# Kernel tuning notes

Measured on AMD Instinct MI355X. Metric: run time of the kernel, lower is better.

## Reference

```python
import jax, jax.numpy as jnp
import numpy as np

NUM_GROUPS = 32
EPS = 1e-6


def setup_inputs() -> dict:
    key = jax.random.key(0)
    ks = jax.random.split(key, 4)
    B, C, H, W = 16, 512, 32, 32
    x = jax.random.normal(ks[0], (B, C, H, W), dtype=jnp.float32)
    norm_w = jnp.ones((C,), dtype=jnp.float32)
    norm_b = jnp.zeros((C,), dtype=jnp.float32)
    qkv_w = jax.random.normal(ks[1], (3 * C, C), dtype=jnp.float32) * (1.0 / np.sqrt(C))
    qkv_b = jnp.zeros((3 * C,), dtype=jnp.float32)
    proj_w = jax.random.normal(ks[2], (C, C), dtype=jnp.float32) * (1.0 / np.sqrt(C))
    proj_b = jnp.zeros((C,), dtype=jnp.float32)
    return {"x": x, "norm_w": norm_w, "norm_b": norm_b, "qkv_w": qkv_w,
            "qkv_b": qkv_b, "proj_w": proj_w, "proj_b": proj_b}


def _group_norm(x, w, b):
    B, C, H, W = x.shape
    g = NUM_GROUPS
    xg = x.reshape(B, g, C // g, H * W)
    mu = xg.mean(axis=(2, 3), keepdims=True)
    var = xg.var(axis=(2, 3), keepdims=True)
    xn = (xg - mu) * jax.lax.rsqrt(var + EPS)
    xn = xn.reshape(B, C, H, W)
    return xn * w[None, :, None, None] + b[None, :, None, None]


def reference(x, norm_w, norm_b, qkv_w, qkv_b, proj_w, proj_b):
    B, C, H, W = x.shape
    h = _group_norm(x, norm_w, norm_b)
    # 1x1 conv == channel GEMM
    qkv = jnp.einsum('oc,bchw->bohw', qkv_w, h) + qkv_b[None, :, None, None]
    q, k, v = jnp.split(qkv, 3, axis=1)
    N = H * W
    q = q.reshape(B, C, N)  # (b, c, n)
    k = k.reshape(B, C, N)
    v = v.reshape(B, C, N)
    scale = jnp.asarray(C, x.dtype) ** -0.5
    attn = jnp.einsum('bci,bcj->bij', q, k) * scale  # (b, Nq, Nk)
    attn = jax.nn.softmax(attn, axis=2)
    o = jnp.einsum('bcj,bij->bci', v, attn).reshape(B, C, H, W)
    out = jnp.einsum('oc,bchw->bohw', proj_w, o) + proj_b[None, :, None, None]
    return x + out
```

## Files before the change

### kernel.cpp

```cpp
#include <hip/hip_runtime.h>

typedef unsigned short u16;
typedef __bf16 bf16x8 __attribute__((ext_vector_type(8)));
typedef float f32x4 __attribute__((ext_vector_type(4)));

#define AS1 __attribute__((address_space(1)))
#define AS3 __attribute__((address_space(3)))


__device__ __forceinline__ u16 f2bf(float f) {
  union { float f; unsigned u; } v; v.f = f;
  return (u16)((v.u + 0x7fffu + ((v.u >> 16) & 1u)) >> 16);
}

__device__ __forceinline__ f32x4 mfma16(bf16x8 a, bf16x8 b, f32x4 c) {
  return __builtin_amdgcn_mfma_f32_16x16x32_bf16(a, b, c, 0, 0, 0);
}

__device__ __forceinline__ void stage_tile(const u16* __restrict__ src, size_t ld,
                                           u16* lds, int wv, int lane) {
#pragma unroll
  for (int h2 = 0; h2 < 2; h2++) {
    int rbase = wv * 32 + h2 * 16;
    int row = rbase + (lane >> 2);
    int segd = (lane & 3) ^ ((row >> 1) & 3);
    __builtin_amdgcn_global_load_lds(
        (const AS1 void*)(src + (size_t)row * ld + segd * 8),
        (AS3 void*)(lds + rbase * 32), 16, 0, 0);
  }
}

__device__ __forceinline__ bf16x8 ldsfrag(const u16* lds, int row, int rowq) {
  int q = rowq ^ ((row >> 1) & 3);
  return *(const bf16x8*)(lds + row * 32 + q * 8);
}

template<int NT>
__device__ __forceinline__ void gemm_core2(const u16* __restrict__ A, int lda,
                                           const u16* __restrict__ B, int ldb,
                                           u16* lds, f32x4 (&acc)[4][4],
                                           int wave, int lane) {
  u16* sA0 = lds;        u16* sA1 = lds + 4096;
  u16* sB0 = lds + 8192; u16* sB1 = lds + 12288;
  int wm = wave >> 1, wn = wave & 1;
  int col = lane & 15, rq = lane >> 4;
#pragma unroll
  for (int m = 0; m < 4; m++)
#pragma unroll
    for (int n = 0; n < 4; n++) acc[m][n] = (f32x4){0.f, 0.f, 0.f, 0.f};

  stage_tile(A, lda, sA0, wave, lane);
  stage_tile(B, ldb, sB0, wave, lane);
  stage_tile(A + 32, lda, sA1, wave, lane);
  stage_tile(B + 32, ldb, sB1, wave, lane);

  for (int t = 0; t < NT; t++) {
    u16* cA = (t & 1) ? sA1 : sA0;
    u16* cB = (t & 1) ? sB1 : sB0;
    if (t < NT - 1) {
      asm volatile("s_waitcnt vmcnt(4)" ::: "memory");
    } else {
      asm volatile("s_waitcnt vmcnt(0)" ::: "memory");
    }
    __builtin_amdgcn_sched_barrier(0);
    __builtin_amdgcn_s_barrier();
    __builtin_amdgcn_sched_barrier(0);
    bf16x8 af[4], bfr[4];
#pragma unroll
    for (int n = 0; n < 4; n++) bfr[n] = ldsfrag(cB, wn * 64 + n * 16 + col, rq);
#pragma unroll
    for (int m = 0; m < 4; m++) af[m] = ldsfrag(cA, wm * 64 + m * 16 + col, rq);
#pragma unroll
    for (int m = 0; m < 4; m++)
#pragma unroll
      for (int n = 0; n < 4; n++) acc[m][n] = mfma16(af[m], bfr[n], acc[m][n]);
    __builtin_amdgcn_sched_barrier(0);
    __builtin_amdgcn_s_barrier();
    if (t + 2 < NT) {
      stage_tile(A + (size_t)(t + 2) * 32, lda, cA, wave, lane);
      stage_tile(B + (size_t)(t + 2) * 32, ldb, cB, wave, lane);
    }
  }
}

__device__ __forceinline__ void stage_half(const u16* __restrict__ src, size_t ld,
                                           u16* ldsbase, int wave, int lane) {
#pragma unroll
  for (int r = 0; r < 2; r++) {
    int rb = (r * 8 + wave) * 8;
    int row = rb + (lane >> 3);
    int seg = (lane & 7) ^ (row & 7);
    __builtin_amdgcn_global_load_lds(
        (const AS1 void*)(src + (size_t)row * ld + seg * 8),
        (AS3 void*)(ldsbase + rb * 64), 16, 0, 0);
  }
}

template<int P>
__device__ __forceinline__ void phase_read(const u16* cA, const u16* cB,
                                           bf16x8 (&af)[2][2], bf16x8 (&bfr)[4][2],
                                           int wm, int wn, int col, int rq) {
  if constexpr (P == 0) {
#pragma unroll
    for (int nf = 0; nf < 4; nf++)
#pragma unroll
      for (int kk = 0; kk < 2; kk++) {
        int row = wn * 64 + nf * 16 + col;
        bfr[nf][kk] = *(const bf16x8*)(cB + row * 64 + (((kk << 2) + rq) ^ (row & 7)) * 8);
      }
  }
#pragma unroll
  for (int i = 0; i < 2; i++)
#pragma unroll
    for (int kk = 0; kk < 2; kk++) {
      int row = wm * 128 + (P * 2 + i) * 16 + col;
      af[i][kk] = *(const bf16x8*)(cA + row * 64 + (((kk << 2) + rq) ^ (row & 7)) * 8);
    }
}

template<int P>
__device__ __forceinline__ void phase_fma(const bf16x8 (&af)[2][2],
                                          const bf16x8 (&bfr)[4][2],
                                          f32x4 (&acc)[8][4]) {
#pragma unroll
  for (int i = 0; i < 2; i++)
#pragma unroll
    for (int kk = 0; kk < 2; kk++)
#pragma unroll
      for (int nf = 0; nf < 4; nf++)
        acc[P * 2 + i][nf] = mfma16(af[i][kk], bfr[nf][kk], acc[P * 2 + i][nf]);
}

#define RUN_PHASE(P, STAGE_CODE, WAIT_CODE)                                  \
  {                                                                          \
    bf16x8 af[2][2];                                                         \
    phase_read<P>(cA, cB, af, bfr, wm, wn, col, rq);                         \
    STAGE_CODE;                                                              \
    WAIT_CODE;                                                               \
    __builtin_amdgcn_sched_barrier(0);                                       \
    __builtin_amdgcn_s_barrier();                                            \
    __builtin_amdgcn_sched_barrier(0);                                       \
    __builtin_amdgcn_s_setprio(1);                                           \
    phase_fma<P>(af, bfr, acc);                                              \
    __builtin_amdgcn_s_setprio(0);                                           \
    __builtin_amdgcn_sched_barrier(0);                                       \
    __builtin_amdgcn_s_barrier();                                            \
    __builtin_amdgcn_sched_barrier(0);                                       \
  }

template<int NT>
__device__ __forceinline__ void gemm8_core(const u16* __restrict__ A, int lda,
                                           const u16* __restrict__ B, int ldb,
                                           u16* lds, f32x4 (&acc)[8][4],
                                           int wave, int lane) {
  u16* Abuf[2] = {lds, lds + 16384};
  u16* Bbuf[2] = {lds + 32768, lds + 49152};
  int wm = wave >> 2, wn = wave & 3;
  int col = lane & 15, rq = lane >> 4;
#pragma unroll
  for (int m = 0; m < 8; m++)
#pragma unroll
    for (int n = 0; n < 4; n++) acc[m][n] = (f32x4){0.f, 0.f, 0.f, 0.f};

  stage_half(A, lda, Abuf[0], wave, lane);
  stage_half(A + 128 * (size_t)lda, lda, Abuf[0] + 8192, wave, lane);
  stage_half(B, ldb, Bbuf[0], wave, lane);
  stage_half(B + 128 * (size_t)ldb, ldb, Bbuf[0] + 8192, wave, lane);
  stage_half(B + 64, ldb, Bbuf[1], wave, lane);
  stage_half(B + 64 + 128 * (size_t)ldb, ldb, Bbuf[1] + 8192, wave, lane);
  asm volatile("s_waitcnt vmcnt(4)" ::: "memory");
  __builtin_amdgcn_sched_barrier(0);
  __builtin_amdgcn_s_barrier();
  __builtin_amdgcn_sched_barrier(0);

  for (int kt = 0; kt < NT; kt++) {
    const u16* cA = Abuf[kt & 1];
    const u16* cB = Bbuf[kt & 1];
    u16* nA = Abuf[(kt + 1) & 1];
    u16* nB = Bbuf[kt & 1];
    const u16* Asrc = A + (size_t)(kt + 1) * 64;
    const u16* Bsrc = B + (size_t)(kt + 2) * 64;
    bool pa = (kt + 1 < NT), pb = (kt + 2 < NT);
    bf16x8 bfr[4][2];
    RUN_PHASE(0, if (pa) stage_half(Asrc, lda, nA, wave, lane), );
    RUN_PHASE(1, if (pa) stage_half(Asrc + 128 * (size_t)lda, lda, nA + 8192, wave, lane), );
    RUN_PHASE(2, if (pb) stage_half(Bsrc, ldb, nB, wave, lane), );
    RUN_PHASE(3, if (pb) stage_half(Bsrc + 128 * (size_t)ldb, ldb, nB + 8192, wave, lane),
              if (pb) { asm volatile("s_waitcnt vmcnt(4)" ::: "memory"); }
              else    { asm volatile("s_waitcnt vmcnt(0)" ::: "memory"); });
  }
}

__global__ __launch_bounds__(256) void gn_fused(const float* __restrict__ x,
                                                const float* __restrict__ gw,
                                                const float* __restrict__ gb,
                                                u16* __restrict__ h) {
  __shared__ float buf[16 * 1032];
  __shared__ float ls[4], lss[4];
  int bg = blockIdx.x;
  int b = bg >> 5, g = bg & 31;
  const float4* p = (const float4*)(x + (size_t)bg * 16384);
  float s = 0.f, ss = 0.f;
  for (int i = threadIdx.x; i < 4096; i += 256) {
    float4 v = p[i];
    int c = i >> 8, n = (i & 255) * 4;
    *(float4*)&buf[c * 1032 + n] = v;
    s  += v.x + v.y + v.z + v.w;
    ss += v.x*v.x + v.y*v.y + v.z*v.z + v.w*v.w;
  }
  for (int d = 32; d; d >>= 1) { s += __shfl_down(s, d); ss += __shfl_down(ss, d); }
  int wv = threadIdx.x >> 6;
  if ((threadIdx.x & 63) == 0) { ls[wv] = s; lss[wv] = ss; }
  __syncthreads();
  float m = (ls[0] + ls[1] + ls[2] + ls[3]) * (1.f / 16384.f);
  float var = (lss[0] + lss[1] + lss[2] + lss[3]) * (1.f / 16384.f) - m * m;
  float r = rsqrtf(var + 1e-6f);
  int c0 = g * 16;
  float w[16], bb[16];
#pragma unroll
  for (int c = 0; c < 16; c++) {
    w[c] = gw[c0 + c] * r;
    bb[c] = gb[c0 + c] - m * w[c];
  }
  for (int n = threadIdx.x; n < 1024; n += 256) {
    u16 o[16];
#pragma unroll
    for (int c = 0; c < 16; c++) o[c] = f2bf(buf[c * 1032 + n] * w[c] + bb[c]);
    u16* dst = h + (((size_t)((b << 10) | n)) << 9) + c0;
    *(uint4*)dst = *(uint4*)o;
    *(uint4*)(dst + 8) = *(uint4*)(o + 8);
  }
}

__global__ __launch_bounds__(256) void cast_w(const float* __restrict__ qkv_w,
                                              const float* __restrict__ proj_w,
                                              u16* __restrict__ wq,
                                              u16* __restrict__ wp) {
  int bid = blockIdx.x;
  const float* src = (bid < 768) ? qkv_w : proj_w;
  u16* dst = (bid < 768) ? wq : wp;
  int base = (bid < 768) ? bid * 1024 : (bid - 768) * 1024;
  int i = base + threadIdx.x * 4;
  float4 v = *(const float4*)(src + i);
  dst[i] = f2bf(v.x); dst[i+1] = f2bf(v.y); dst[i+2] = f2bf(v.z); dst[i+3] = f2bf(v.w);
}

__global__ __launch_bounds__(512, 1) void gemm8_qkv(const u16* __restrict__ A,
                                                    const u16* __restrict__ Bn,
                                                    const float* __restrict__ bias,
                                                    u16* __restrict__ q_nc,
                                                    u16* __restrict__ k_nc,
                                                    u16* __restrict__ v) {
  __shared__ u16 lds[65536];
  int bid = blockIdx.x;
  int xcd = bid & 7, r = bid >> 3;
  int mb = r % 6, nb = xcd * 8 + r / 6;
  int m0 = mb * 256, n0 = nb * 256;
  int t = threadIdx.x, wave = t >> 6, lane = t & 63;
  int wm = wave >> 2, wn = wave & 3;
  int col = lane & 15, rq = lane >> 4;
  f32x4 acc[8][4];
  gemm8_core<8>(A + (size_t)m0 * 512, 512, Bn + (size_t)n0 * 512, 512,
                lds, acc, wave, lane);
  if (mb < 4) {
    u16* dst = (mb < 2) ? q_nc : k_nc;
#pragma unroll
    for (int mf = 0; mf < 8; mf++)
#pragma unroll
      for (int nf = 0; nf < 4; nf++) {
        int o = m0 + wm * 128 + mf * 16 + rq * 4;
        int bn = n0 + wn * 64 + nf * 16 + col;
        u16 tmp[4];
#pragma unroll
        for (int rr = 0; rr < 4; rr++) tmp[rr] = f2bf(acc[mf][nf][rr] + bias[o + rr]);
        *(uint2*)(dst + (size_t)bn * 512 + (o & 511)) = *(uint2*)tmp;
      }
  } else {
#pragma unroll
    for (int mf = 0; mf < 8; mf++)
#pragma unroll
      for (int nf = 0; nf < 4; nf++)
#pragma unroll
        for (int rr = 0; rr < 4; rr++) {
          int o = m0 + wm * 128 + mf * 16 + rq * 4 + rr;
          int bn = n0 + wn * 64 + nf * 16 + col;
          v[(size_t)(o & 511) * 16384 + bn] = f2bf(acc[mf][nf][rr] + bias[o]);
        }
  }
}

__global__ __launch_bounds__(512, 1) void gemm8_s(const u16* __restrict__ q_nc,
                                                  const u16* __restrict__ k_nc,
                                                  u16* __restrict__ E,
                                                  float* __restrict__ part) {
  __shared__ u16 lds[65536];
  int bid = blockIdx.x;
  int xcd = bid & 7, r = bid >> 3;
  int b = xcd * 2 + (r & 1);
  int tile = r >> 1;
  int m0 = (tile >> 2) * 256, n0 = (tile & 3) * 256;
  int t = threadIdx.x, wave = t >> 6, lane = t & 63;
  int wm = wave >> 2, wn = wave & 3;
  int col = lane & 15, rq = lane >> 4;
  f32x4 acc[8][4];
  gemm8_core<8>(q_nc + ((size_t)(b * 1024 + m0)) * 512, 512,
                k_nc + ((size_t)(b * 1024 + n0)) * 512, 512,
                lds, acc, wave, lane);
  u16* Eb = E + ((size_t)b << 20);
  float* pb = part + ((size_t)b << 14);
  int idx = (n0 >> 6) + wn;
  const float scale = 0.04419417382415922f;
#pragma unroll
  for (int mf = 0; mf < 8; mf++)
#pragma unroll
    for (int rr = 0; rr < 4; rr++) {
      float e[4], rs = 0.f;
#pragma unroll
      for (int nf = 0; nf < 4; nf++) { e[nf] = __expf(acc[mf][nf][rr] * scale); rs += e[nf]; }
      rs += __shfl_xor(rs, 1); rs += __shfl_xor(rs, 2);
      rs += __shfl_xor(rs, 4); rs += __shfl_xor(rs, 8);
      int row = m0 + wm * 128 + mf * 16 + rq * 4 + rr;
      if (col == 0) pb[row * 16 + idx] = rs;
#pragma unroll
      for (int nf = 0; nf < 4; nf++) {
        int jj = n0 + wn * 64 + nf * 16 + col;
        Eb[(size_t)row * 1024 + jj] = f2bf(e[nf]);
      }
    }
}

__global__ __launch_bounds__(256) void row_inv2(const float* __restrict__ part,
                                                float* __restrict__ inv) {
  int row = blockIdx.x * 256 + threadIdx.x;
  const float4* p = (const float4*)(part + (size_t)row * 16);
  float4 a = p[0], b = p[1], c = p[2], d = p[3];
  float s = a.x+a.y+a.z+a.w + b.x+b.y+b.z+b.w + c.x+c.y+c.z+c.w + d.x+d.y+d.z+d.w;
  inv[row] = 1.f / s;
}

__global__ __launch_bounds__(256) void gemm_pv(const u16* __restrict__ E,
                                               const u16* __restrict__ v,
                                               const float* __restrict__ inv,
                                               u16* __restrict__ o_nc) {
  __shared__ u16 lds[16384];
  int bid = blockIdx.x;
  int xcd = bid & 7, r = bid >> 3;
  int b = xcd * 2 + (r & 1);
  int tile = r >> 1;
  int m0 = (tile >> 2) * 128, n0 = (tile & 3) * 128;
  int t = threadIdx.x, wave = t >> 6, lane = t & 63;
  int wm = wave >> 1, wn = wave & 1;
  int col = lane & 15, rq = lane >> 4;
  f32x4 acc[4][4];
  gemm_core2<32>(E + ((size_t)b << 20) + (size_t)m0 * 1024, 1024,
                 v + (size_t)n0 * 16384 + ((size_t)b << 10), 16384,
                 lds, acc, wave, lane);
#pragma unroll
  for (int i = 0; i < 4; i++)
#pragma unroll
    for (int rr = 0; rr < 4; rr++) {
      int ii = m0 + wm * 64 + i * 16 + rq * 4 + rr;
      float sc = inv[(b << 10) + ii];
#pragma unroll
      for (int j = 0; j < 4; j++) {
        int cc = n0 + wn * 64 + j * 16 + col;
        o_nc[(((size_t)(b * 1024 + ii)) << 9) + cc] = f2bf(acc[i][j][rr] * sc);
      }
    }
}

__global__ __launch_bounds__(256) void gemm_proj(const u16* __restrict__ A,
                                                 const u16* __restrict__ Bn,
                                                 const float* __restrict__ bias,
                                                 const float* __restrict__ xres,
                                                 float* __restrict__ outp) {
  __shared__ u16 lds[16384];
  int bid = blockIdx.x;
  int xcd = bid & 7, r = bid >> 3;
  int mb = r & 3, nb = xcd * 16 + (r >> 2);
  int m0 = mb * 128, n0 = nb * 128;
  int t = threadIdx.x, wave = t >> 6, lane = t & 63;
  int wm = wave >> 1, wn = wave & 1;
  int col = lane & 15, rq = lane >> 4;
  f32x4 acc[4][4];
  gemm_core2<16>(A + (size_t)m0 * 512, 512, Bn + (size_t)n0 * 512, 512,
                 lds, acc, wave, lane);
#pragma unroll
  for (int i = 0; i < 4; i++)
#pragma unroll
    for (int j = 0; j < 4; j++)
#pragma unroll
      for (int rr = 0; rr < 4; rr++) {
        int co = m0 + wm * 64 + i * 16 + rq * 4 + rr;
        int bn = n0 + wn * 64 + j * 16 + col;
        int bb = bn >> 10, n = bn & 1023;
        size_t oi = (((size_t)(bb * 512 + co)) << 10) + n;
        outp[oi] = acc[i][j][rr] + bias[co] + xres[oi];
      }
}

extern "C" void kernel_launch(void* const* d_in, const int* in_sizes, int n_in,
                              void* d_out, int out_size, void* d_ws, size_t ws_size,
                              hipStream_t stream) {
  const float* x      = (const float*)d_in[0];
  const float* norm_w = (const float*)d_in[1];
  const float* norm_b = (const float*)d_in[2];
  const float* qkv_w  = (const float*)d_in[3];
  const float* qkv_b  = (const float*)d_in[4];
  const float* proj_w = (const float*)d_in[5];
  const float* proj_b = (const float*)d_in[6];
  float* out = (float*)d_out;

  char* ws = (char*)d_ws;
  size_t off = 0;
  auto alloc = [&](size_t bytes) {
    void* p = ws + off;
    off += (bytes + 255) & ~(size_t)255;
    return p;
  };
  float* part = (float*)alloc((size_t)16384 * 16 * 4);
  float* inv  = (float*)alloc(16384 * 4);
  u16* wq   = (u16*)alloc((size_t)1536 * 512 * 2);
  u16* wp   = (u16*)alloc((size_t)512 * 512 * 2);
  u16* h    = (u16*)alloc((size_t)16384 * 512 * 2);
  u16* q_nc = (u16*)alloc((size_t)16384 * 512 * 2);
  u16* k_nc = (u16*)alloc((size_t)16384 * 512 * 2);
  u16* v    = (u16*)alloc((size_t)512 * 16384 * 2);
  u16* E    = (u16*)alloc((size_t)16 * 1024 * 1024 * 2);
  u16* o_nc = h;
  (void)in_sizes; (void)n_in; (void)out_size; (void)ws_size;

  gn_fused<<<512, 256, 0, stream>>>(x, norm_w, norm_b, h);
  cast_w<<<1024, 256, 0, stream>>>(qkv_w, proj_w, wq, wp);
  gemm8_qkv<<<384, 512, 0, stream>>>(wq, h, qkv_b, q_nc, k_nc, v);
  gemm8_s<<<256, 512, 0, stream>>>(q_nc, k_nc, E, part);
  row_inv2<<<64, 256, 0, stream>>>(part, inv);
  gemm_pv<<<512, 256, 0, stream>>>(E, v, inv, o_nc);
  gemm_proj<<<512, 256, 0, stream>>>(wp, o_nc, proj_b, x, out);
}
```

Baseline: 138.6 us.

## Fuse weight cast and row-inverse kernels, stage GEMM epilogues through LDS

Folds the bf16 weight cast into the group-norm kernel and the softmax row-sum inversion into the PV GEMM, which removes two kernel launches. The QKV GEMM moves from 256x256 tiles with 512 threads to 128x128 tiles with 256 threads at higher occupancy. The QKV, S, and PV epilogues now stage results in LDS (padded or XOR-swizzled) and write them out as coalesced 16-byte stores instead of scattered 2-byte or 8-byte stores. The cost is extra LDS traffic and barriers, plus smaller QKV tiles that give less data reuse.

```diff
diff --git a/kernel.cpp b/kernel.cpp
--- a/kernel.cpp
+++ b/kernel.cpp
@@ -80,6 +80,16 @@
       stage_tile(A + (size_t)(t + 2) * 32, lda, cA, wave, lane);
       stage_tile(B + (size_t)(t + 2) * 32, ldb, cB, wave, lane);
     }
+  }
+}
+
+__device__ __forceinline__ void epi_flush(const u16* lds, u16* gdst, size_t stride, int t) {
+#pragma unroll
+  for (int pass = 0; pass < 8; pass++) {
+    int row = pass * 16 + (t >> 4);
+    int ch = (t & 15) * 8;
+    uint4 w = *(const uint4*)(lds + row * 132 + ch);
+    *(uint4*)(gdst + (size_t)row * stride + ch) = w;
   }
 }
 
@@ -194,7 +204,11 @@
 __global__ __launch_bounds__(256) void gn_fused(const float* __restrict__ x,
                                                 const float* __restrict__ gw,
                                                 const float* __restrict__ gb,
-                                                u16* __restrict__ h) {
+                                                const float* __restrict__ qkv_w,
+                                                const float* __restrict__ proj_w,
+                                                u16* __restrict__ h,
+                                                u16* __restrict__ wq,
+                                                u16* __restrict__ wp) {
   __shared__ float buf[16 * 1032];
   __shared__ float ls[4], lss[4];
   int bg = blockIdx.x;
@@ -208,6 +222,20 @@
     s  += v.x + v.y + v.z + v.w;
     ss += v.x*v.x + v.y*v.y + v.z*v.z + v.w*v.w;
   }
+  {
+    int qb = bg * 384;
+    for (int u = threadIdx.x; u < 384; u += 256) {
+      float4 v = *(const float4*)(qkv_w + (size_t)(qb + u) * 4);
+      int o = (qb + u) * 4;
+      wq[o] = f2bf(v.x); wq[o+1] = f2bf(v.y); wq[o+2] = f2bf(v.z); wq[o+3] = f2bf(v.w);
+    }
+    int pb = bg * 128;
+    if (threadIdx.x < 128) {
+      float4 v = *(const float4*)(proj_w + (size_t)(pb + threadIdx.x) * 4);
+      int o = (pb + threadIdx.x) * 4;
+      wp[o] = f2bf(v.x); wp[o+1] = f2bf(v.y); wp[o+2] = f2bf(v.z); wp[o+3] = f2bf(v.w);
+    }
+  }
   for (int d = 32; d; d >>= 1) { s += __shfl_down(s, d); ss += __shfl_down(ss, d); }
   int wv = threadIdx.x >> 6;
   if ((threadIdx.x & 63) == 0) { ls[wv] = s; lss[wv] = ss; }
@@ -232,60 +260,55 @@
   }
 }
 
-__global__ __launch_bounds__(256) void cast_w(const float* __restrict__ qkv_w,
-                                              const float* __restrict__ proj_w,
-                                              u16* __restrict__ wq,
-                                              u16* __restrict__ wp) {
-  int bid = blockIdx.x;
-  const float* src = (bid < 768) ? qkv_w : proj_w;
-  u16* dst = (bid < 768) ? wq : wp;
-  int base = (bid < 768) ? bid * 1024 : (bid - 768) * 1024;
-  int i = base + threadIdx.x * 4;
-  float4 v = *(const float4*)(src + i);
-  dst[i] = f2bf(v.x); dst[i+1] = f2bf(v.y); dst[i+2] = f2bf(v.z); dst[i+3] = f2bf(v.w);
-}
-
-__global__ __launch_bounds__(512, 1) void gemm8_qkv(const u16* __restrict__ A,
-                                                    const u16* __restrict__ Bn,
-                                                    const float* __restrict__ bias,
-                                                    u16* __restrict__ q_nc,
-                                                    u16* __restrict__ k_nc,
-                                                    u16* __restrict__ v) {
-  __shared__ u16 lds[65536];
+__global__ __launch_bounds__(256, 4) void gemm_qkv(const u16* __restrict__ A,
+                                                   const u16* __restrict__ Bn,
+                                                   const float* __restrict__ bias,
+                                                   u16* __restrict__ q_nc,
+                                                   u16* __restrict__ k_nc,
+                                                   u16* __restrict__ v) {
+  __shared__ u16 lds[16896];
   int bid = blockIdx.x;
   int xcd = bid & 7, r = bid >> 3;
-  int mb = r % 6, nb = xcd * 8 + r / 6;
-  int m0 = mb * 256, n0 = nb * 256;
+  int mb = r % 12, nb = xcd * 16 + r / 12;
+  int m0 = mb * 128, n0 = nb * 128;
   int t = threadIdx.x, wave = t >> 6, lane = t & 63;
-  int wm = wave >> 2, wn = wave & 3;
-  int col = lane & 15, rq = lane >> 4;
-  f32x4 acc[8][4];
-  gemm8_core<8>(A + (size_t)m0 * 512, 512, Bn + (size_t)n0 * 512, 512,
-                lds, acc, wave, lane);
-  if (mb < 4) {
-    u16* dst = (mb < 2) ? q_nc : k_nc;
-#pragma unroll
-    for (int mf = 0; mf < 8; mf++)
-#pragma unroll
-      for (int nf = 0; nf < 4; nf++) {
-        int o = m0 + wm * 128 + mf * 16 + rq * 4;
-        int bn = n0 + wn * 64 + nf * 16 + col;
+  int wm = wave >> 1, wn = wave & 1;
+  int col = lane & 15, rq = lane >> 4;
+  f32x4 acc[4][4];
+  gemm_core2<16>(A + (size_t)m0 * 512, 512, Bn + (size_t)n0 * 512, 512,
+                 lds, acc, wave, lane);
+  __syncthreads();
+  if (mb < 8) {
+#pragma unroll
+    for (int i = 0; i < 4; i++)
+#pragma unroll
+      for (int j = 0; j < 4; j++) {
+        int o = m0 + wm * 64 + i * 16 + rq * 4;
         u16 tmp[4];
 #pragma unroll
-        for (int rr = 0; rr < 4; rr++) tmp[rr] = f2bf(acc[mf][nf][rr] + bias[o + rr]);
-        *(uint2*)(dst + (size_t)bn * 512 + (o & 511)) = *(uint2*)tmp;
+        for (int rr = 0; rr < 4; rr++) tmp[rr] = f2bf(acc[i][j][rr] + bias[o + rr]);
+        int bnl = wn * 64 + j * 16 + col;
+        int chl = wm * 64 + i * 16 + rq * 4;
+        *(uint2*)(lds + bnl * 132 + chl) = *(uint2*)tmp;
       }
+    __syncthreads();
+    u16* dst = ((mb < 4) ? q_nc : k_nc) + (size_t)n0 * 512 + (m0 & 511);
+    epi_flush(lds, dst, 512, t);
   } else {
 #pragma unroll
-    for (int mf = 0; mf < 8; mf++)
-#pragma unroll
-      for (int nf = 0; nf < 4; nf++)
+    for (int i = 0; i < 4; i++)
+#pragma unroll
+      for (int j = 0; j < 4; j++)
 #pragma unroll
         for (int rr = 0; rr < 4; rr++) {
-          int o = m0 + wm * 128 + mf * 16 + rq * 4 + rr;
-          int bn = n0 + wn * 64 + nf * 16 + col;
-          v[(size_t)(o & 511) * 16384 + bn] = f2bf(acc[mf][nf][rr] + bias[o]);
+          int o = m0 + wm * 64 + i * 16 + rq * 4 + rr;
+          int chl = wm * 64 + i * 16 + rq * 4 + rr;
+          int bnl = wn * 64 + j * 16 + col;
+          lds[chl * 132 + bnl] = f2bf(acc[i][j][rr] + bias[o]);
         }
+    __syncthreads();
+    u16* dst = v + (size_t)(m0 - 1024) * 16384 + n0;
+    epi_flush(lds, dst, 16384, t);
   }
 }
 
@@ -306,10 +329,10 @@
   gemm8_core<8>(q_nc + ((size_t)(b * 1024 + m0)) * 512, 512,
                 k_nc + ((size_t)(b * 1024 + n0)) * 512, 512,
                 lds, acc, wave, lane);
-  u16* Eb = E + ((size_t)b << 20);
   float* pb = part + ((size_t)b << 14);
   int idx = (n0 >> 6) + wn;
   const float scale = 0.04419417382415922f;
+  __syncthreads();
 #pragma unroll
   for (int mf = 0; mf < 8; mf++)
 #pragma unroll
@@ -319,30 +342,33 @@
       for (int nf = 0; nf < 4; nf++) { e[nf] = __expf(acc[mf][nf][rr] * scale); rs += e[nf]; }
       rs += __shfl_xor(rs, 1); rs += __shfl_xor(rs, 2);
       rs += __shfl_xor(rs, 4); rs += __shfl_xor(rs, 8);
-      int row = m0 + wm * 128 + mf * 16 + rq * 4 + rr;
-      if (col == 0) pb[row * 16 + idx] = rs;
+      int il = wm * 128 + mf * 16 + rq * 4 + rr;
+      if (col == 0) pb[(m0 + il) * 16 + idx] = rs;
 #pragma unroll
       for (int nf = 0; nf < 4; nf++) {
-        int jj = n0 + wn * 64 + nf * 16 + col;
-        Eb[(size_t)row * 1024 + jj] = f2bf(e[nf]);
+        int j = wn * 64 + nf * 16 + col;
+        int jb = (j >> 3) ^ (il & 7);
+        lds[il * 256 + (jb << 3) + (j & 7)] = f2bf(e[nf]);
       }
     }
-}
-
-__global__ __launch_bounds__(256) void row_inv2(const float* __restrict__ part,
-                                                float* __restrict__ inv) {
-  int row = blockIdx.x * 256 + threadIdx.x;
-  const float4* p = (const float4*)(part + (size_t)row * 16);
-  float4 a = p[0], b = p[1], c = p[2], d = p[3];
-  float s = a.x+a.y+a.z+a.w + b.x+b.y+b.z+b.w + c.x+c.y+c.z+c.w + d.x+d.y+d.z+d.w;
-  inv[row] = 1.f / s;
-}
-
-__global__ __launch_bounds__(256) void gemm_pv(const u16* __restrict__ E,
-                                               const u16* __restrict__ v,
-                                               const float* __restrict__ inv,
-                                               u16* __restrict__ o_nc) {
-  __shared__ u16 lds[16384];
+  __syncthreads();
+  u16* Eb = E + ((size_t)b << 20) + (size_t)m0 * 1024 + n0;
+#pragma unroll
+  for (int pass = 0; pass < 16; pass++) {
+    int row = pass * 16 + (t >> 5);
+    int jbl = t & 31;
+    uint4 w = *(const uint4*)(lds + row * 256 + (jbl << 3));
+    int jb = jbl ^ (row & 7);
+    *(uint4*)(Eb + (size_t)row * 1024 + (jb << 3)) = w;
+  }
+}
+
+__global__ __launch_bounds__(256, 4) void gemm_pv(const u16* __restrict__ E,
+                                                  const u16* __restrict__ v,
+                                                  const float* __restrict__ part,
+                                                  u16* __restrict__ o_nc) {
+  __shared__ u16 lds[16896];
+  __shared__ float invs[128];
   int bid = blockIdx.x;
   int xcd = bid & 7, r = bid >> 3;
   int b = xcd * 2 + (r & 1);
@@ -355,25 +381,32 @@
   gemm_core2<32>(E + ((size_t)b << 20) + (size_t)m0 * 1024, 1024,
                  v + (size_t)n0 * 16384 + ((size_t)b << 10), 16384,
                  lds, acc, wave, lane);
+  if (t < 128) {
+    const float4* p = (const float4*)(part + ((size_t)((b << 10) + m0 + t)) * 16);
+    float4 a = p[0], bq = p[1], c = p[2], d = p[3];
+    float s = a.x+a.y+a.z+a.w + bq.x+bq.y+bq.z+bq.w + c.x+c.y+c.z+c.w + d.x+d.y+d.z+d.w;
+    invs[t] = 1.f / s;
+  }
+  __syncthreads();
 #pragma unroll
   for (int i = 0; i < 4; i++)
 #pragma unroll
     for (int rr = 0; rr < 4; rr++) {
-      int ii = m0 + wm * 64 + i * 16 + rq * 4 + rr;
-      float sc = inv[(b << 10) + ii];
-#pragma unroll
-      for (int j = 0; j < 4; j++) {
-        int cc = n0 + wn * 64 + j * 16 + col;
-        o_nc[(((size_t)(b * 1024 + ii)) << 9) + cc] = f2bf(acc[i][j][rr] * sc);
-      }
-    }
-}
-
-__global__ __launch_bounds__(256) void gemm_proj(const u16* __restrict__ A,
-                                                 const u16* __restrict__ Bn,
-                                                 const float* __restrict__ bias,
-                                                 const float* __restrict__ xres,
-                                                 float* __restrict__ outp) {
+      int iil = wm * 64 + i * 16 + rq * 4 + rr;
+      float sc = invs[iil];
+#pragma unroll
+      for (int j = 0; j < 4; j++)
+        lds[iil * 132 + wn * 64 + j * 16 + col] = f2bf(acc[i][j][rr] * sc);
+    }
+  __syncthreads();
+  epi_flush(lds, o_nc + ((size_t)(b * 1024 + m0)) * 512 + n0, 512, t);
+}
+
+__global__ __launch_bounds__(256, 4) void gemm_proj(const u16* __restrict__ A,
+                                                    const u16* __restrict__ Bn,
+                                                    const float* __restrict__ bias,
+                                                    const float* __restrict__ xres,
+                                                    float* __restrict__ outp) {
   __shared__ u16 lds[16384];
   int bid = blockIdx.x;
   int xcd = bid & 7, r = bid >> 3;
@@ -419,7 +452,6 @@
     return p;
   };
   float* part = (float*)alloc((size_t)16384 * 16 * 4);
-  float* inv  = (float*)alloc(16384 * 4);
   u16* wq   = (u16*)alloc((size_t)1536 * 512 * 2);
   u16* wp   = (u16*)alloc((size_t)512 * 512 * 2);
   u16* h    = (u16*)alloc((size_t)16384 * 512 * 2);
@@ -430,11 +462,9 @@
   u16* o_nc = h;
   (void)in_sizes; (void)n_in; (void)out_size; (void)ws_size;
 
-  gn_fused<<<512, 256, 0, stream>>>(x, norm_w, norm_b, h);
-  cast_w<<<1024, 256, 0, stream>>>(qkv_w, proj_w, wq, wp);
-  gemm8_qkv<<<384, 512, 0, stream>>>(wq, h, qkv_b, q_nc, k_nc, v);
+  gn_fused<<<512, 256, 0, stream>>>(x, norm_w, norm_b, qkv_w, proj_w, h, wq, wp);
+  gemm_qkv<<<1536, 256, 0, stream>>>(wq, h, qkv_b, q_nc, k_nc, v);
   gemm8_s<<<256, 512, 0, stream>>>(q_nc, k_nc, E, part);
-  row_inv2<<<64, 256, 0, stream>>>(part, inv);
-  gemm_pv<<<512, 256, 0, stream>>>(E, v, inv, o_nc);
+  gemm_pv<<<512, 256, 0, stream>>>(E, v, part, o_nc);
   gemm_proj<<<512, 256, 0, stream>>>(wp, o_nc, proj_b, x, out);
 }
```

New measurement: 132.3 us. -4.5%, faster.
